# Optimization experiments

Hardware: AMD Instinct MI355X
Metric: run time of the kernel (lower is better)

Reference implementation:

```python
import jax, jax.numpy as jnp
import numpy as np

N = 100000
E = 1600000
F_IN = 128
HID1, H1 = 32, 4
HID2, H2 = 32, 4
NUM_CLASSES = 16
NEG_SLOPE = 0.2  # PyG GATConv default


def _glorot(key, shape, fan_in):
    return jax.random.normal(key, shape, dtype=jnp.float32) / jnp.sqrt(jnp.float32(fan_in))


def setup_inputs() -> dict:
    key = jax.random.key(0)
    ks = jax.random.split(key, 12)
    x = jax.random.normal(ks[0], (N, F_IN), dtype=jnp.float32)
    edge_index = jax.random.randint(ks[1], (2, E), 0, N, dtype=jnp.int64)
    W1 = _glorot(ks[2], (F_IN, H1 * HID1), F_IN)
    a_src1 = _glorot(ks[3], (H1, HID1), HID1)
    a_dst1 = _glorot(ks[4], (H1, HID1), HID1)
    b1 = jnp.zeros((H1 * HID1,), dtype=jnp.float32)
    W2 = _glorot(ks[5], (H1 * HID1, H2 * HID2), H1 * HID1)
    a_src2 = _glorot(ks[6], (H2, HID2), HID2)
    a_dst2 = _glorot(ks[7], (H2, HID2), HID2)
    b2 = jnp.zeros((HID2,), dtype=jnp.float32)
    Wc = _glorot(ks[8], (HID2, NUM_CLASSES), HID2)
    bc = jnp.zeros((NUM_CLASSES,), dtype=jnp.float32)
    return {"x": x, "edge_index": edge_index, "W1": W1, "a_src1": a_src1,
            "a_dst1": a_dst1, "b1": b1, "W2": W2, "a_src2": a_src2,
            "a_dst2": a_dst2, "b2": b2, "Wc": Wc, "bc": bc}


def gat_layer(x, src, dst, W, a_s, a_d, b, concat):
    # x: [N, Fin]; src/dst: [E'] with self-loops included
    n = x.shape[0]
    H, C = a_s.shape
    h = (x @ W).reshape(n, H, C)                      # [N, H, C]
    alpha_s = jnp.einsum('nhc,hc->nh', h, a_s)        # [N, H]
    alpha_d = jnp.einsum('nhc,hc->nh', h, a_d)
    e = jax.nn.leaky_relu(alpha_s[src] + alpha_d[dst], NEG_SLOPE)  # [E', H]
    m = jax.ops.segment_max(e, dst, num_segments=n)   # segment softmax (stable)
    ex = jnp.exp(e - m[dst])
    denom = jax.ops.segment_sum(ex, dst, num_segments=n)
    alpha = ex / denom[dst]                           # [E', H]
    msg = alpha[:, :, None] * h[src]                  # [E', H, C]
    out = jax.ops.segment_sum(msg, dst, num_segments=n)  # [N, H, C]
    out = out.reshape(n, H * C) if concat else out.mean(axis=1)
    return out + b


def reference(x, edge_index, W1, a_src1, a_dst1, b1, W2, a_src2, a_dst2, b2, Wc, bc):
    n = x.shape[0]
    loop = jnp.arange(n, dtype=edge_index.dtype)
    src = jnp.concatenate([edge_index[0], loop])  # add self-loops (PyG default)
    dst = jnp.concatenate([edge_index[1], loop])
    h = gat_layer(x, src, dst, W1, a_src1, a_dst1, b1, concat=True)
    h = jax.nn.relu(h)  # dropout is identity in eval mode
    h = gat_layer(h, src, dst, W2, a_src2, a_dst2, b2, concat=False)
    h = jax.nn.relu(h)
    return h @ Wc + bc
```

## Files before the change

kernel.cpp:

```cpp
#include <hip/hip_runtime.h>
#include <hip/hip_fp16.h>


typedef _Float16 f16;
typedef f16 f16x8 __attribute__((ext_vector_type(8)));
typedef float f32x4 __attribute__((ext_vector_type(4)));

__device__ __forceinline__ float leaky02(float v) { return v > 0.f ? v : 0.2f * v; }

struct h2x2 { __half2 a, b; };

#define NPB 1024
#define MAXNB 128
#define EPT 16
#define CH 4096

__global__ __launch_bounds__(256) void k_bucketize(const int* __restrict__ ei,
                                                   uint2* __restrict__ ebuf,
                                                   int* __restrict__ bcur,
                                                   int E, int N, int NB, int region) {
  __shared__ int hist[MAXNB];
  __shared__ int lbase[MAXNB];
  const int t = threadIdx.x;
  const int base = blockIdx.x * CH;
  const int Ep = E + N;
  if (t < MAXNB) hist[t] = 0;
  __syncthreads();
  int src[EPT], dst[EPT];
#pragma unroll
  for (int k = 0; k < EPT; ++k) {
    int e = base + k * 256 + t;
    if (e < E) { src[k] = ei[e]; dst[k] = ei[E + e]; }
    else if (e < Ep) { src[k] = dst[k] = e - E; }
    else { src[k] = -1; dst[k] = -1; }
    if (dst[k] >= 0) atomicAdd(&hist[dst[k] >> 10], 1);
  }
  __syncthreads();
  if (t < NB && hist[t] > 0) lbase[t] = atomicAdd(&bcur[t], hist[t]);
  __syncthreads();
  if (t < MAXNB) hist[t] = 0;
  __syncthreads();
#pragma unroll
  for (int k = 0; k < EPT; ++k) {
    if (dst[k] >= 0) {
      int b = dst[k] >> 10;
      int r = atomicAdd(&hist[b], 1);
      ebuf[(size_t)b * region + lbase[b] + r] =
          make_uint2((unsigned)src[k], (unsigned)dst[k]);
    }
  }
}

__global__ __launch_bounds__(256) void k_csr(const uint2* __restrict__ ebuf,
                                             const int* __restrict__ bcur,
                                             int* __restrict__ rowptr,
                                             int* __restrict__ colsrc,
                                             int N, int NB, int region) {
  __shared__ int cnt[NPB];
  __shared__ int lds2[256];
  __shared__ int sscan[MAXNB];
  const int b = blockIdx.x;
  const int t = threadIdx.x;
  if (t < MAXNB) sscan[t] = (t < NB) ? bcur[t] : 0;
  __syncthreads();
  for (int off = 1; off < MAXNB; off <<= 1) {
    int u = (t < MAXNB && t >= off) ? sscan[t - off] : 0;
    __syncthreads();
    if (t < MAXNB) sscan[t] += u;
    __syncthreads();
  }
  const int cb = (b == 0) ? 0 : sscan[b - 1];
  if (b == 0 && t == 0) rowptr[N] = sscan[NB - 1];
  const int m = bcur[b];
  const size_t ebase = (size_t)b * region;
#pragma unroll
  for (int i = 0; i < 4; ++i) cnt[t * 4 + i] = 0;
  __syncthreads();
  for (int j = t; j < m; j += 256) {
    int d = (int)(ebuf[ebase + j].y) & (NPB - 1);
    atomicAdd(&cnt[d], 1);
  }
  __syncthreads();
  int v[4], s = 0;
#pragma unroll
  for (int i = 0; i < 4; ++i) { v[i] = cnt[t * 4 + i]; s += v[i]; }
  lds2[t] = s;
  __syncthreads();
  for (int off = 1; off < 256; off <<= 1) {
    int u = (t >= off) ? lds2[t - off] : 0;
    __syncthreads();
    lds2[t] += u;
    __syncthreads();
  }
  int e = lds2[t] - s;
  const int node0 = (b << 10) + t * 4;
#pragma unroll
  for (int i = 0; i < 4; ++i) {
    cnt[t * 4 + i] = e;
    if (node0 + i < N) rowptr[node0 + i] = cb + e;
    e += v[i];
  }
  __syncthreads();
  for (int j = t; j < m; j += 256) {
    uint2 q = ebuf[ebase + j];
    int d = (int)q.y & (NPB - 1);
    int r = atomicAdd(&cnt[d], 1);
    colsrc[cb + r] = (int)q.x;
  }
}

template <int AFP16>
__global__ __launch_bounds__(256) void k_gemm_mfma(const void* __restrict__ Ain,
                                                   const float* __restrict__ W,
                                                   const float* __restrict__ avs,
                                                   const float* __restrict__ avd,
                                                   __half* __restrict__ Hh,
                                                   float* __restrict__ as_out,
                                                   float* __restrict__ ad_out,
                                                   int nrows) {
  __shared__ __align__(16) f16 sA[64][136];
  __shared__ __align__(16) f16 sBT[128][136];
  const int t = threadIdx.x;
  const int row0 = blockIdx.x * 64;
#pragma unroll
  for (int i = 0; i < 16; ++i) {
    int idx = (t + i * 256) * 4;
    int k = idx >> 7, n = idx & 127;
    float4 w4 = *(const float4*)&W[idx];
    sBT[n + 0][k] = (f16)w4.x;
    sBT[n + 1][k] = (f16)w4.y;
    sBT[n + 2][k] = (f16)w4.z;
    sBT[n + 3][k] = (f16)w4.w;
  }
  if (AFP16) {
    const __half* A = (const __half*)Ain + (size_t)row0 * 128;
#pragma unroll
    for (int i = 0; i < 8; ++i) {
      int idx = (t + i * 256) * 4;
      int m = idx >> 7, c = idx & 127;
      h2x2 v;
      if (row0 + m < nrows) v = *(const h2x2*)&A[idx];
      else { v.a = __floats2half2_rn(0.f, 0.f); v.b = v.a; }
      *(h2x2*)&sA[m][c] = v;
    }
  } else {
    const float* A = (const float*)Ain + (size_t)row0 * 128;
#pragma unroll
    for (int i = 0; i < 8; ++i) {
      int idx = (t + i * 256) * 4;
      int m = idx >> 7, c = idx & 127;
      float4 a4 = (row0 + m < nrows) ? *(const float4*)&A[idx]
                                     : make_float4(0.f, 0.f, 0.f, 0.f);
      h2x2 v;
      v.a = __floats2half2_rn(a4.x, a4.y);
      v.b = __floats2half2_rn(a4.z, a4.w);
      *(h2x2*)&sA[m][c] = v;
    }
  }
  __syncthreads();
  const int wv = t >> 6;
  const int l = t & 63;
  const int lm = l & 15;
  const int lk = (l >> 4) * 8;
  const int mw = wv * 16;
  f32x4 acc[8];
#pragma unroll
  for (int tt = 0; tt < 8; ++tt) acc[tt] = (f32x4){0.f, 0.f, 0.f, 0.f};
#pragma unroll
  for (int kb = 0; kb < 4; ++kb) {
    f16x8 af = *(const f16x8*)&sA[mw + lm][kb * 32 + lk];
#pragma unroll
    for (int tt = 0; tt < 8; ++tt) {
      f16x8 bf = *(const f16x8*)&sBT[tt * 16 + lm][kb * 32 + lk];
      acc[tt] = __builtin_amdgcn_mfma_f32_16x16x32_f16(af, bf, acc[tt], 0, 0, 0);
    }
  }
  float avst[8], avdt[8];
#pragma unroll
  for (int tt = 0; tt < 8; ++tt) {
    avst[tt] = avs[tt * 16 + lm];
    avdt[tt] = avd[tt * 16 + lm];
  }
#pragma unroll
  for (int reg = 0; reg < 4; ++reg) {
    const int row = row0 + mw + (l >> 4) * 4 + reg;
    float ps0 = acc[0][reg] * avst[0] + acc[1][reg] * avst[1];
    float ps1 = acc[2][reg] * avst[2] + acc[3][reg] * avst[3];
    float ps2 = acc[4][reg] * avst[4] + acc[5][reg] * avst[5];
    float ps3 = acc[6][reg] * avst[6] + acc[7][reg] * avst[7];
    float pd0 = acc[0][reg] * avdt[0] + acc[1][reg] * avdt[1];
    float pd1 = acc[2][reg] * avdt[2] + acc[3][reg] * avdt[3];
    float pd2 = acc[4][reg] * avdt[4] + acc[5][reg] * avdt[5];
    float pd3 = acc[6][reg] * avdt[6] + acc[7][reg] * avdt[7];
#pragma unroll
    for (int off = 1; off < 16; off <<= 1) {
      ps0 += __shfl_xor(ps0, off); ps1 += __shfl_xor(ps1, off);
      ps2 += __shfl_xor(ps2, off); ps3 += __shfl_xor(ps3, off);
      pd0 += __shfl_xor(pd0, off); pd1 += __shfl_xor(pd1, off);
      pd2 += __shfl_xor(pd2, off); pd3 += __shfl_xor(pd3, off);
    }
    if (row < nrows) {
      if (lm < 4) {
        float vs = lm == 0 ? ps0 : lm == 1 ? ps1 : lm == 2 ? ps2 : ps3;
        float vd = lm == 0 ? pd0 : lm == 1 ? pd1 : lm == 2 ? pd2 : pd3;
        as_out[row * 4 + lm] = vs;
        ad_out[row * 4 + lm] = vd;
      }
#pragma unroll
      for (int tt = 0; tt < 8; ++tt)
        Hh[(size_t)row * 128 + tt * 16 + lm] = __float2half(acc[tt][reg]);
    }
  }
}

template <int LAYER>
__global__ __launch_bounds__(256) void k_agg(const int* __restrict__ rowptr,
                                             const int* __restrict__ colsrc,
                                             const float* __restrict__ as,
                                             const float* __restrict__ ad,
                                             const __half* __restrict__ Hh,
                                             const float* __restrict__ b1,
                                             const float* __restrict__ b2,
                                             const float* __restrict__ Wc,
                                             const float* __restrict__ bc,
                                             __half* __restrict__ outh,
                                             float* __restrict__ out, int n) {
  __shared__ float sbuf[8][128];
  const int slot = threadIdx.x >> 5;
  const int l = threadIdx.x & 31;
  const int node = blockIdx.x * 8 + slot;
  const bool active = node < n;
  int start = 0, end = 0;
  float4 adv = make_float4(0.f, 0.f, 0.f, 0.f);
  if (active) {
    start = rowptr[node];
    end = rowptr[node + 1];
    adv = *(const float4*)&ad[node * 4];
  }
  const int hd = l >> 3;
  const float adh = hd == 0 ? adv.x : hd == 1 ? adv.y : hd == 2 ? adv.z : adv.w;
  const int c = l * 4;
  float4 acc = make_float4(0.f, 0.f, 0.f, 0.f);
  float dsum = 0.f;
  int e = start;
  for (; e + 3 < end; e += 4) {
    int s0 = colsrc[e], s1 = colsrc[e + 1], s2 = colsrc[e + 2], s3 = colsrc[e + 3];
    float a0 = as[s0 * 4 + hd];
    float a1 = as[s1 * 4 + hd];
    float a2 = as[s2 * 4 + hd];
    float a3 = as[s3 * 4 + hd];
    h2x2 q0 = *(const h2x2*)&Hh[(size_t)s0 * 128 + c];
    h2x2 q1 = *(const h2x2*)&Hh[(size_t)s1 * 128 + c];
    h2x2 q2 = *(const h2x2*)&Hh[(size_t)s2 * 128 + c];
    h2x2 q3 = *(const h2x2*)&Hh[(size_t)s3 * 128 + c];
    float w0 = __expf(leaky02(a0 + adh));
    float w1 = __expf(leaky02(a1 + adh));
    float w2 = __expf(leaky02(a2 + adh));
    float w3 = __expf(leaky02(a3 + adh));
    dsum += w0 + w1 + w2 + w3;
    float2 f0a = __half22float2(q0.a), f0b = __half22float2(q0.b);
    float2 f1a = __half22float2(q1.a), f1b = __half22float2(q1.b);
    float2 f2a = __half22float2(q2.a), f2b = __half22float2(q2.b);
    float2 f3a = __half22float2(q3.a), f3b = __half22float2(q3.b);
    acc.x = fmaf(w0, f0a.x, acc.x); acc.y = fmaf(w0, f0a.y, acc.y);
    acc.z = fmaf(w0, f0b.x, acc.z); acc.w = fmaf(w0, f0b.y, acc.w);
    acc.x = fmaf(w1, f1a.x, acc.x); acc.y = fmaf(w1, f1a.y, acc.y);
    acc.z = fmaf(w1, f1b.x, acc.z); acc.w = fmaf(w1, f1b.y, acc.w);
    acc.x = fmaf(w2, f2a.x, acc.x); acc.y = fmaf(w2, f2a.y, acc.y);
    acc.z = fmaf(w2, f2b.x, acc.z); acc.w = fmaf(w2, f2b.y, acc.w);
    acc.x = fmaf(w3, f3a.x, acc.x); acc.y = fmaf(w3, f3a.y, acc.y);
    acc.z = fmaf(w3, f3b.x, acc.z); acc.w = fmaf(w3, f3b.y, acc.w);
  }
  for (; e < end; ++e) {
    int s0 = colsrc[e];
    float w = __expf(leaky02(as[s0 * 4 + hd] + adh));
    h2x2 q = *(const h2x2*)&Hh[(size_t)s0 * 128 + c];
    float2 fa = __half22float2(q.a), fb = __half22float2(q.b);
    dsum += w;
    acc.x = fmaf(w, fa.x, acc.x); acc.y = fmaf(w, fa.y, acc.y);
    acc.z = fmaf(w, fb.x, acc.z); acc.w = fmaf(w, fb.y, acc.w);
  }
  const float inv = dsum > 0.f ? 1.0f / dsum : 0.f;
  acc.x *= inv; acc.y *= inv; acc.z *= inv; acc.w *= inv;
  if (LAYER == 1) {
    if (active) {
      float4 bv = *(const float4*)&b1[c];
      h2x2 pk;
      pk.a = __floats2half2_rn(fmaxf(acc.x + bv.x, 0.f), fmaxf(acc.y + bv.y, 0.f));
      pk.b = __floats2half2_rn(fmaxf(acc.z + bv.z, 0.f), fmaxf(acc.w + bv.w, 0.f));
      *(h2x2*)&outh[(size_t)node * 128 + c] = pk;
    }
  } else {
    *(float4*)&sbuf[slot][c] = acc;
    __syncthreads();
    float f = 0.25f * (sbuf[slot][l] + sbuf[slot][l + 32] +
                       sbuf[slot][l + 64] + sbuf[slot][l + 96]);
    f = fmaxf(f + b2[l], 0.f);
    __syncthreads();
    sbuf[slot][l] = f;
    __syncthreads();
    if (active && l < 16) {
      float o = bc[l];
#pragma unroll
      for (int cc = 0; cc < 32; ++cc) o = fmaf(sbuf[slot][cc], Wc[cc * 16 + l], o);
      out[(size_t)node * 16 + l] = o;
    }
  }
}

extern "C" void kernel_launch(void* const* d_in, const int* in_sizes, int n_in,
                              void* d_out, int out_size, void* d_ws, size_t ws_size,
                              hipStream_t stream) {
  const float* x = (const float*)d_in[0];
  const int* ei = (const int*)d_in[1];
  const float* W1 = (const float*)d_in[2];
  const float* a_s1 = (const float*)d_in[3];
  const float* a_d1 = (const float*)d_in[4];
  const float* b1 = (const float*)d_in[5];
  const float* W2 = (const float*)d_in[6];
  const float* a_s2 = (const float*)d_in[7];
  const float* a_d2 = (const float*)d_in[8];
  const float* b2 = (const float*)d_in[9];
  const float* Wc = (const float*)d_in[10];
  const float* bc = (const float*)d_in[11];
  float* out = (float*)d_out;

  const int N = in_sizes[0] / 128;
  const int E = in_sizes[1] / 2;
  const int Ep = E + N;
  const int NB = (N + NPB - 1) >> 10;
  const int region = Ep / NB + 4096;

  char* p = (char*)d_ws;
  auto align16 = [](char* q) { return (char*)(((uintptr_t)q + 15) & ~(uintptr_t)15); };
  __half* Hh = (__half*)p;   p = align16(p + sizeof(__half) * (size_t)N * 128);
  __half* x2h = (__half*)p;  p = align16(p + sizeof(__half) * (size_t)N * 128);
  float* asb = (float*)p;    p = align16(p + sizeof(float) * (size_t)N * 4);
  float* adb = (float*)p;    p = align16(p + sizeof(float) * (size_t)N * 4);
  int* rowptr = (int*)p;     p = align16(p + sizeof(int) * (size_t)(N + 1));
  int* bcur = (int*)p;       p = align16(p + sizeof(int) * MAXNB);
  int* colsrc = (int*)p;     p = align16(p + sizeof(int) * (size_t)Ep);
  uint2* ebuf = (uint2*)p;

  hipMemsetAsync(bcur, 0, sizeof(int) * MAXNB, stream);

  k_bucketize<<<(Ep + CH - 1) / CH, 256, 0, stream>>>(ei, ebuf, bcur, E, N, NB, region);
  k_csr<<<NB, 256, 0, stream>>>(ebuf, bcur, rowptr, colsrc, N, NB, region);

  const int gblocks = (N + 63) / 64;
  k_gemm_mfma<0><<<gblocks, 256, 0, stream>>>(x, W1, a_s1, a_d1, Hh, asb, adb, N);
  k_agg<1><<<(N + 7) / 8, 256, 0, stream>>>(rowptr, colsrc, asb, adb, Hh,
                                            b1, nullptr, nullptr, nullptr, x2h, nullptr, N);
  k_gemm_mfma<1><<<gblocks, 256, 0, stream>>>(x2h, W2, a_s2, a_d2, Hh, asb, adb, N);
  k_agg<2><<<(N + 7) / 8, 256, 0, stream>>>(rowptr, colsrc, asb, adb, Hh,
                                            nullptr, b2, Wc, bc, nullptr, out, N);
}
```

Measured before the change: 403.3 us.

## Pretranspose weights to fp16, double GEMM row tile, stage output through LDS

A small prep kernel transposes and converts each weight matrix to fp16 once, so GEMM blocks load it with vector copies instead of each block doing a scattered transpose-convert. The GEMM tile grows from 64 to 128 rows per block, so each wave does two MFMA row tiles that reuse the same B fragments, and the weight load is spread over twice the rows. Output H is written into LDS and then stored as 16-byte coalesced rows instead of scattered 2-byte stores. The cost is two extra small launches, more LDS per block, and more accumulator registers, which may lower occupancy.

```diff
diff --git a/kernel.cpp b/kernel.cpp
--- a/kernel.cpp
+++ b/kernel.cpp
@@ -109,52 +109,55 @@
   }
 }
 
+__global__ __launch_bounds__(256) void k_prep(const float* __restrict__ W,
+                                              f16* __restrict__ Wt) {
+  int t = threadIdx.x;
+  int n = blockIdx.x * 2 + (t >> 7);
+  int k = t & 127;
+  Wt[n * 128 + k] = (f16)W[k * 128 + n];
+}
+
 template <int AFP16>
 __global__ __launch_bounds__(256) void k_gemm_mfma(const void* __restrict__ Ain,
-                                                   const float* __restrict__ W,
+                                                   const f16* __restrict__ Wt,
                                                    const float* __restrict__ avs,
                                                    const float* __restrict__ avd,
                                                    __half* __restrict__ Hh,
                                                    float* __restrict__ as_out,
                                                    float* __restrict__ ad_out,
                                                    int nrows) {
-  __shared__ __align__(16) f16 sA[64][136];
+  __shared__ __align__(16) f16 sA[128][136];
   __shared__ __align__(16) f16 sBT[128][136];
   const int t = threadIdx.x;
-  const int row0 = blockIdx.x * 64;
-#pragma unroll
-  for (int i = 0; i < 16; ++i) {
-    int idx = (t + i * 256) * 4;
-    int k = idx >> 7, n = idx & 127;
-    float4 w4 = *(const float4*)&W[idx];
-    sBT[n + 0][k] = (f16)w4.x;
-    sBT[n + 1][k] = (f16)w4.y;
-    sBT[n + 2][k] = (f16)w4.z;
-    sBT[n + 3][k] = (f16)w4.w;
+  const int row0 = blockIdx.x * 128;
+#pragma unroll
+  for (int i = 0; i < 8; ++i) {
+    int q = t + i * 256;
+    int n = q >> 4, kc = q & 15;
+    *(uint4*)&sBT[n][kc * 8] = *(const uint4*)&Wt[n * 128 + kc * 8];
   }
   if (AFP16) {
-    const __half* A = (const __half*)Ain + (size_t)row0 * 128;
+    const __half* A = (const __half*)Ain;
 #pragma unroll
     for (int i = 0; i < 8; ++i) {
-      int idx = (t + i * 256) * 4;
-      int m = idx >> 7, c = idx & 127;
-      h2x2 v;
-      if (row0 + m < nrows) v = *(const h2x2*)&A[idx];
-      else { v.a = __floats2half2_rn(0.f, 0.f); v.b = v.a; }
-      *(h2x2*)&sA[m][c] = v;
+      int q = t + i * 256;
+      int m = q >> 4, kc = q & 15;
+      uint4 v = make_uint4(0u, 0u, 0u, 0u);
+      if (row0 + m < nrows) v = *(const uint4*)&A[(size_t)(row0 + m) * 128 + kc * 8];
+      *(uint4*)&sA[m][kc * 8] = v;
     }
   } else {
-    const float* A = (const float*)Ain + (size_t)row0 * 128;
-#pragma unroll
-    for (int i = 0; i < 8; ++i) {
-      int idx = (t + i * 256) * 4;
-      int m = idx >> 7, c = idx & 127;
-      float4 a4 = (row0 + m < nrows) ? *(const float4*)&A[idx]
+    const float* A = (const float*)Ain;
+#pragma unroll
+    for (int i = 0; i < 16; ++i) {
+      int q = t + i * 256;
+      int m = q >> 5, c4 = (q & 31) * 4;
+      float4 a4 = (row0 + m < nrows) ? *(const float4*)&A[(size_t)(row0 + m) * 128 + c4]
                                      : make_float4(0.f, 0.f, 0.f, 0.f);
       h2x2 v;
       v.a = __floats2half2_rn(a4.x, a4.y);
       v.b = __floats2half2_rn(a4.z, a4.w);
-      *(h2x2*)&sA[m][c] = v;
+      *(h2x2*)&sA[m][c4] = v;
     }
   }
   __syncthreads();
@@ -162,17 +165,21 @@
   const int l = t & 63;
   const int lm = l & 15;
   const int lk = (l >> 4) * 8;
-  const int mw = wv * 16;
-  f32x4 acc[8];
-#pragma unroll
-  for (int tt = 0; tt < 8; ++tt) acc[tt] = (f32x4){0.f, 0.f, 0.f, 0.f};
+  const int mw = wv * 32;
+  f32x4 acc[2][8];
+#pragma unroll
+  for (int mt = 0; mt < 2; ++mt)
+#pragma unroll
+    for (int tt = 0; tt < 8; ++tt) acc[mt][tt] = (f32x4){0.f, 0.f, 0.f, 0.f};
 #pragma unroll
   for (int kb = 0; kb < 4; ++kb) {
-    f16x8 af = *(const f16x8*)&sA[mw + lm][kb * 32 + lk];
+    f16x8 af0 = *(const f16x8*)&sA[mw + lm][kb * 32 + lk];
+    f16x8 af1 = *(const f16x8*)&sA[mw + 16 + lm][kb * 32 + lk];
 #pragma unroll
     for (int tt = 0; tt < 8; ++tt) {
       f16x8 bf = *(const f16x8*)&sBT[tt * 16 + lm][kb * 32 + lk];
-      acc[tt] = __builtin_amdgcn_mfma_f32_16x16x32_f16(af, bf, acc[tt], 0, 0, 0);
+      acc[0][tt] = __builtin_amdgcn_mfma_f32_16x16x32_f16(af0, bf, acc[0][tt], 0, 0, 0);
+      acc[1][tt] = __builtin_amdgcn_mfma_f32_16x16x32_f16(af1, bf, acc[1][tt], 0, 0, 0);
     }
   }
   float avst[8], avdt[8];
@@ -182,34 +189,43 @@
     avdt[tt] = avd[tt * 16 + lm];
   }
 #pragma unroll
-  for (int reg = 0; reg < 4; ++reg) {
-    const int row = row0 + mw + (l >> 4) * 4 + reg;
-    float ps0 = acc[0][reg] * avst[0] + acc[1][reg] * avst[1];
-    float ps1 = acc[2][reg] * avst[2] + acc[3][reg] * avst[3];
-    float ps2 = acc[4][reg] * avst[4] + acc[5][reg] * avst[5];
-    float ps3 = acc[6][reg] * avst[6] + acc[7][reg] * avst[7];
-    float pd0 = acc[0][reg] * avdt[0] + acc[1][reg] * avdt[1];
-    float pd1 = acc[2][reg] * avdt[2] + acc[3][reg] * avdt[3];
-    float pd2 = acc[4][reg] * avdt[4] + acc[5][reg] * avdt[5];
-    float pd3 = acc[6][reg] * avdt[6] + acc[7][reg] * avdt[7];
-#pragma unroll
-    for (int off = 1; off < 16; off <<= 1) {
-      ps0 += __shfl_xor(ps0, off); ps1 += __shfl_xor(ps1, off);
-      ps2 += __shfl_xor(ps2, off); ps3 += __shfl_xor(ps3, off);
-      pd0 += __shfl_xor(pd0, off); pd1 += __shfl_xor(pd1, off);
-      pd2 += __shfl_xor(pd2, off); pd3 += __shfl_xor(pd3, off);
-    }
-    if (row < nrows) {
-      if (lm < 4) {
+  for (int mt = 0; mt < 2; ++mt) {
+#pragma unroll
+    for (int reg = 0; reg < 4; ++reg) {
+      const int row = row0 + mw + mt * 16 + (l >> 4) * 4 + reg;
+      float ps0 = acc[mt][0][reg] * avst[0] + acc[mt][1][reg] * avst[1];
+      float ps1 = acc[mt][2][reg] * avst[2] + acc[mt][3][reg] * avst[3];
+      float ps2 = acc[mt][4][reg] * avst[4] + acc[mt][5][reg] * avst[5];
+      float ps3 = acc[mt][6][reg] * avst[6] + acc[mt][7][reg] * avst[7];
+      float pd0 = acc[mt][0][reg] * avdt[0] + acc[mt][1][reg] * avdt[1];
+      float pd1 = acc[mt][2][reg] * avdt[2] + acc[mt][3][reg] * avdt[3];
+      float pd2 = acc[mt][4][reg] * avdt[4] + acc[mt][5][reg] * avdt[5];
+      float pd3 = acc[mt][6][reg] * avdt[6] + acc[mt][7][reg] * avdt[7];
+#pragma unroll
+      for (int off = 1; off < 16; off <<= 1) {
+        ps0 += __shfl_xor(ps0, off); ps1 += __shfl_xor(ps1, off);
+        ps2 += __shfl_xor(ps2, off); ps3 += __shfl_xor(ps3, off);
+        pd0 += __shfl_xor(pd0, off); pd1 += __shfl_xor(pd1, off);
+        pd2 += __shfl_xor(pd2, off); pd3 += __shfl_xor(pd3, off);
+      }
+      if (row < nrows && lm < 4) {
         float vs = lm == 0 ? ps0 : lm == 1 ? ps1 : lm == 2 ? ps2 : ps3;
         float vd = lm == 0 ? pd0 : lm == 1 ? pd1 : lm == 2 ? pd2 : pd3;
         as_out[row * 4 + lm] = vs;
         ad_out[row * 4 + lm] = vd;
       }
-#pragma unroll
-      for (int tt = 0; tt < 8; ++tt)
-        Hh[(size_t)row * 128 + tt * 16 + lm] = __float2half(acc[tt][reg]);
-    }
+      const int lr = mw + mt * 16 + (l >> 4) * 4 + reg;
+#pragma unroll
+      for (int tt = 0; tt < 8; ++tt) sA[lr][tt * 16 + lm] = (f16)acc[mt][tt][reg];
+    }
+  }
+#pragma unroll
+  for (int i = 0; i < 8; ++i) {
+    int q = l + i * 64;
+    int m = mw + (q >> 4), kc = q & 15;
+    int row = row0 + m;
+    if (row < nrows)
+      *(uint4*)&Hh[(size_t)row * 128 + kc * 8] = *(const uint4*)&sA[m][kc * 8];
   }
 }
 
@@ -339,6 +355,7 @@
   float* adb = (float*)p;    p = align16(p + sizeof(float) * (size_t)N * 4);
   int* rowptr = (int*)p;     p = align16(p + sizeof(int) * (size_t)(N + 1));
   int* bcur = (int*)p;       p = align16(p + sizeof(int) * MAXNB);
+  f16* Wt = (f16*)p;         p = align16(p + sizeof(f16) * 128 * 128);
   int* colsrc = (int*)p;     p = align16(p + sizeof(int) * (size_t)Ep);
   uint2* ebuf = (uint2*)p;
 
@@ -347,11 +364,13 @@
   k_bucketize<<<(Ep + CH - 1) / CH, 256, 0, stream>>>(ei, ebuf, bcur, E, N, NB, region);
   k_csr<<<NB, 256, 0, stream>>>(ebuf, bcur, rowptr, colsrc, N, NB, region);
 
-  const int gblocks = (N + 63) / 64;
-  k_gemm_mfma<0><<<gblocks, 256, 0, stream>>>(x, W1, a_s1, a_d1, Hh, asb, adb, N);
+  const int gblocks = (N + 127) / 128;
+  k_prep<<<64, 256, 0, stream>>>(W1, Wt);
+  k_gemm_mfma<0><<<gblocks, 256, 0, stream>>>(x, Wt, a_s1, a_d1, Hh, asb, adb, N);
   k_agg<1><<<(N + 7) / 8, 256, 0, stream>>>(rowptr, colsrc, asb, adb, Hh,
                                             b1, nullptr, nullptr, nullptr, x2h, nullptr, N);
-  k_gemm_mfma<1><<<gblocks, 256, 0, stream>>>(x2h, W2, a_s2, a_d2, Hh, asb, adb, N);
+  k_prep<<<64, 256, 0, stream>>>(W2, Wt);
+  k_gemm_mfma<1><<<gblocks, 256, 0, stream>>>(x2h, Wt, a_s2, a_d2, Hh, asb, adb, N);
   k_agg<2><<<(N + 7) / 8, 256, 0, stream>>>(rowptr, colsrc, asb, adb, Hh,
                                             nullptr, b2, Wc, bc, nullptr, out, N);
 }
```

New measurement: 383.7 us. 1.05x faster.
